# Performance work log

Hardware: AMD Instinct MI355X
Metric: run time of the kernel (lower is better)

The kernel has to match this reference:

```python
import jax, jax.numpy as jnp
import numpy as np

BLOCK = 128          # quantization block size
F8_MAX = 448.0       # max representable magnitude of float8_e4m3fn


def setup_inputs() -> dict:
    key = jax.random.key(0)
    k1, k2, k3 = jax.random.split(key, 3)
    M, K, N = 8192, 4096, 4096
    Kb, Nb = K // BLOCK, N // BLOCK
    x = jax.random.normal(k1, (M, K), jnp.float32)
    # weight stored as fp8-representable values (simulated with f32 container)
    weight = jax.random.normal(k2, (N, K), jnp.float32)
    # per 128x128-block weight dequant scales (positive, small, like amax/448)
    weight_scale = jax.random.uniform(k3, (Nb, Kb), jnp.float32, 0.5, 1.5) * 0.01
    return {"x": x, "weight": weight, "weight_scale": weight_scale}


def _act_quant(x):
    """fp8_blockwise_act_quant: per-(row, 128-block) scale = amax/448, cast to e4m3."""
    M, K = x.shape
    Kb = K // BLOCK
    xb = x.reshape(M, Kb, BLOCK)
    amax = jnp.max(jnp.abs(xb), axis=-1, keepdims=True)            # [M, Kb, 1]
    scale = jnp.maximum(amax, 1e-12) / F8_MAX                      # [M, Kb, 1]
    xq = (xb / scale).astype(jnp.float8_e4m3fn).astype(jnp.float32)
    return xq, scale


def reference(x, weight, weight_scale):
    # ---- activation blockwise fp8 quant ----
    xq, x_scale = _act_quant(x)                                    # [M,Kb,B], [M,Kb,1]
    M, Kb, _ = xq.shape
    K = Kb * BLOCK
    x_deq = (xq * x_scale).reshape(M, K)                           # dequantized activations

    # ---- weight blockwise fp8 dequant (weight stored as fp8 values) ----
    N = weight.shape[0]
    Nb = N // BLOCK
    wq = weight.astype(jnp.float8_e4m3fn).astype(jnp.float32)      # fp8 storage
    w_deq = (wq.reshape(Nb, BLOCK, Kb, BLOCK)
             * weight_scale[:, None, :, None]).reshape(N, K)

    # ---- scaled GEMM: y = x_deq @ w_deq^T (bias is None) ----
    return x_deq @ w_deq.T                                         # [M, N]
```

## Files before the change

### kernel.cpp

```cpp
#include <hip/hip_runtime.h>


typedef int   v4i __attribute__((ext_vector_type(4)));
typedef int   v8i __attribute__((ext_vector_type(8)));
typedef float v4f __attribute__((ext_vector_type(4)));

constexpr int M  = 8192;
constexpr int K  = 4096;
constexpr int N  = 4096;
constexpr int KB = K / 128;
constexpr int NB = N / 128;

constexpr int XBLOCKS = (M * KB * 8) / 256;
constexpr int WBLOCKS = (int)(((long long)N * K / 16) / 256);

#define GLOBAL_AS __attribute__((address_space(1)))
#define LDS_AS    __attribute__((address_space(3)))

__device__ __forceinline__ void async16(const void* g, void* l) {
  __builtin_amdgcn_global_load_lds((const GLOBAL_AS void*)g, (LDS_AS void*)l, 16, 0, 0);
}


__global__ __launch_bounds__(256) void quant_fused_kernel(
    const float* __restrict__ x, const float* __restrict__ w,
    unsigned char* __restrict__ xq, unsigned char* __restrict__ wq,
    float* __restrict__ xs_t ) {
  const int tid = threadIdx.x;
  if (blockIdx.x < XBLOCKS) {
    const long long blk = ((long long)blockIdx.x * 256 + tid) >> 3;
    const int s = tid & 7;
    const int m  = (int)(blk >> 5);
    const int kb = (int)(blk & (KB - 1));

    const float4* px = (const float4*)(x + blk * 128 + s * 16);
    float4 v0 = px[0], v1 = px[1], v2 = px[2], v3 = px[3];

    float ax = 0.f;
#define AMAX4(v) ax = fmaxf(ax, fmaxf(fmaxf(fabsf(v.x), fabsf(v.y)), fmaxf(fabsf(v.z), fabsf(v.w))))
    AMAX4(v0); AMAX4(v1); AMAX4(v2); AMAX4(v3);
#undef AMAX4
#pragma unroll
    for (int d = 4; d >= 1; d >>= 1) ax = fmaxf(ax, __shfl_xor(ax, d, 8));
    const float scale = fmaxf(ax, 1e-12f) / 448.0f;

    int p0 = 0, p1 = 0, p2 = 0, p3 = 0;
    p0 = __builtin_amdgcn_cvt_pk_fp8_f32(v0.x / scale, v0.y / scale, p0, false);
    p0 = __builtin_amdgcn_cvt_pk_fp8_f32(v0.z / scale, v0.w / scale, p0, true);
    p1 = __builtin_amdgcn_cvt_pk_fp8_f32(v1.x / scale, v1.y / scale, p1, false);
    p1 = __builtin_amdgcn_cvt_pk_fp8_f32(v1.z / scale, v1.w / scale, p1, true);
    p2 = __builtin_amdgcn_cvt_pk_fp8_f32(v2.x / scale, v2.y / scale, p2, false);
    p2 = __builtin_amdgcn_cvt_pk_fp8_f32(v2.z / scale, v2.w / scale, p2, true);
    p3 = __builtin_amdgcn_cvt_pk_fp8_f32(v3.x / scale, v3.y / scale, p3, false);
    p3 = __builtin_amdgcn_cvt_pk_fp8_f32(v3.z / scale, v3.w / scale, p3, true);

    const int q = s >> 1, j = s & 1, rr = m & 15;
    const long long base = ((long long)(m >> 4) * KB + kb) * 2048;
    *(v4i*)(xq + base + j * 1024 + (q * 16 + rr) * 16) = (v4i){p0, p1, p2, p3};

    if (s == 0) xs_t[(long long)kb * M + m] = scale;
  } else {
    const long long t = (long long)(blockIdx.x - XBLOCKS) * 256 + tid;
    const int grp = (int)(t >> 7);
    const int idx = (int)(t & 127);
    const int l = idx >> 1, j = idx & 1;
    const int nf = grp >> 5, kb = grp & (KB - 1);
    const int n = nf * 16 + (l & 15);
    const int k = kb * 128 + (l >> 4) * 32 + j * 16;

    const float4* pw = (const float4*)(w + (long long)n * K + k);
    float4 v0 = pw[0], v1 = pw[1], v2 = pw[2], v3 = pw[3];
    int p0 = 0, p1 = 0, p2 = 0, p3 = 0;
    p0 = __builtin_amdgcn_cvt_pk_fp8_f32(v0.x, v0.y, p0, false);
    p0 = __builtin_amdgcn_cvt_pk_fp8_f32(v0.z, v0.w, p0, true);
    p1 = __builtin_amdgcn_cvt_pk_fp8_f32(v1.x, v1.y, p1, false);
    p1 = __builtin_amdgcn_cvt_pk_fp8_f32(v1.z, v1.w, p1, true);
    p2 = __builtin_amdgcn_cvt_pk_fp8_f32(v2.x, v2.y, p2, false);
    p2 = __builtin_amdgcn_cvt_pk_fp8_f32(v2.z, v2.w, p2, true);
    p3 = __builtin_amdgcn_cvt_pk_fp8_f32(v3.x, v3.y, p3, false);
    p3 = __builtin_amdgcn_cvt_pk_fp8_f32(v3.z, v3.w, p3, true);
    *(v4i*)(wq + (long long)grp * 2048 + j * 1024 + l * 16) = (v4i){p0, p1, p2, p3};
  }
}

__global__ __launch_bounds__(512, 2) void gemm_fp8_kernel(
    const unsigned char* __restrict__ xq, const unsigned char* __restrict__ wq,
    const float* __restrict__ xs_t ,
    const float* __restrict__ wscale ,
    float* __restrict__ out) {
  __shared__ unsigned char Asm[2][16 * 2048];
  __shared__ unsigned char Bsm[2][16 * 2048];
  __shared__ float Ssm[2][256];

  const int tid   = threadIdx.x;
  const int ntile = blockIdx.x;
  const int mtile = blockIdx.y;
  const int wave  = tid >> 6;
  const int lane  = tid & 63;
  const int wm = wave >> 2, wn = wave & 3;
  const int l15 = lane & 15, quad = lane >> 4;

  const float wsv = wscale[(ntile * 2 + (wn >> 1)) * KB + (lane & 31)];

  const unsigned char* pa0 =
      xq + ((long long)(mtile * 16 + wave * 2) * KB) * 2048 + lane * 16;
  const unsigned char* pb0 =
      wq + ((long long)(ntile * 16 + wave * 2) * KB) * 2048 + lane * 16;
  const char* ps0 = (const char*)(xs_t + (long long)mtile * 256) + lane * 16;

  auto STAGE = [&](int nbuf, int kbi) {
    const long long koff = (long long)kbi * 2048;
#pragma unroll
    for (int t = 0; t < 4; ++t)
      async16(pa0 + koff + (long long)(t >> 1) * (KB * 2048) + (t & 1) * 1024,
              &Asm[nbuf][(wave * 2 + (t >> 1)) * 2048 + (t & 1) * 1024]);
#pragma unroll
    for (int t = 0; t < 4; ++t)
      async16(pb0 + koff + (long long)(t >> 1) * (KB * 2048) + (t & 1) * 1024,
              &Bsm[nbuf][(wave * 2 + (t >> 1)) * 2048 + (t & 1) * 1024]);
    if (wave == 0) async16(ps0 + (long long)kbi * (M * 4), &Ssm[nbuf][0]);
  };

  v4f acc[8][4];
#pragma unroll
  for (int f = 0; f < 8; ++f)
#pragma unroll
    for (int g = 0; g < 4; ++g) acc[f][g] = (v4f){0.f, 0.f, 0.f, 0.f};

  const v4f z = (v4f){0.f, 0.f, 0.f, 0.f};

  STAGE(0, 0);

#pragma unroll 1
  for (int kb = 0; kb < KB; ++kb) {
    const int cur = kb & 1;
    if (kb < KB - 1) {
      STAGE(cur ^ 1, kb + 1);
      if (wave == 0) asm volatile("s_waitcnt vmcnt(9)" ::: "memory");
      else           asm volatile("s_waitcnt vmcnt(8)" ::: "memory");
    } else {
      asm volatile("s_waitcnt vmcnt(0)" ::: "memory");
    }
    __builtin_amdgcn_s_barrier();
    asm volatile("" ::: "memory");
    __builtin_amdgcn_sched_barrier(0);

    const float ws =
        __uint_as_float(__builtin_amdgcn_readlane(__float_as_uint(wsv), kb));

    v8i b[4];
#pragma unroll
    for (int g = 0; g < 4; ++g) {
      const unsigned char* pb = Bsm[cur] + (wn * 4 + g) * 2048 + lane * 16;
      v4i lo = *(const v4i*)pb;
      v4i hi = *(const v4i*)(pb + 1024);
      b[g][0] = lo[0]; b[g][1] = lo[1]; b[g][2] = lo[2]; b[g][3] = lo[3];
      b[g][4] = hi[0]; b[g][5] = hi[1]; b[g][6] = hi[2]; b[g][7] = hi[3];
    }

#pragma unroll
    for (int f = 0; f < 8; ++f) {
      const unsigned char* pa = Asm[cur] + (wm * 8 + f) * 2048 + lane * 16;
      v4i lo = *(const v4i*)pa;
      v4i hi = *(const v4i*)(pa + 1024);
      v8i a;
      a[0] = lo[0]; a[1] = lo[1]; a[2] = lo[2]; a[3] = lo[3];
      a[4] = hi[0]; a[5] = hi[1]; a[6] = hi[2]; a[7] = hi[3];
      const v4f sxr = *(const v4f*)&Ssm[cur][wm * 128 + f * 16 + quad * 4];
      const v4f s = sxr * ws;
      v4f p[4];
      __builtin_amdgcn_s_setprio(1);
#pragma unroll
      for (int g = 0; g < 4; ++g) {
        p[g] = __builtin_amdgcn_mfma_scale_f32_16x16x128_f8f6f4(
            a, b[g], z, 0, 0, 0, 0x7f7f7f7f, 0, 0x7f7f7f7f);
      }
      __builtin_amdgcn_s_setprio(0);
#pragma unroll
      for (int g = 0; g < 4; ++g) acc[f][g] += s * p[g];
    }
    __syncthreads();
  }

#pragma unroll
  for (int f = 0; f < 8; ++f) {
#pragma unroll
    for (int r = 0; r < 4; ++r) {
      const long long row = mtile * 256 + wm * 128 + f * 16 + quad * 4 + r;
      float* po = out + row * N + ntile * 256 + wn * 64 + l15;
#pragma unroll
      for (int g = 0; g < 4; ++g) po[g * 16] = acc[f][g][r];
    }
  }
}

extern "C" void kernel_launch(void* const* d_in, const int* in_sizes, int n_in,
                              void* d_out, int out_size, void* d_ws, size_t ws_size,
                              hipStream_t stream) {
  const float* x   = (const float*)d_in[0];
  const float* w   = (const float*)d_in[1];
  const float* wsc = (const float*)d_in[2];
  float* out = (float*)d_out;

  unsigned char* ws = (unsigned char*)d_ws;
  unsigned char* xq = ws;
  unsigned char* wq = ws + (size_t)M * K;
  float* xs_t = (float*)(ws + (size_t)M * K + (size_t)N * K);

  quant_fused_kernel<<<XBLOCKS + WBLOCKS, 256, 0, stream>>>(x, w, xq, wq, xs_t);
  gemm_fp8_kernel<<<dim3(N / 256, M / 256), 512, 0, stream>>>(xq, wq, xs_t, wsc, out);
}
```

Before: 422.9 us.

## Split GEMM k-step into four barrier-separated phases interleaving prefetch with MFMA clusters

The main loop of the fp8 GEMM is rebuilt as four phases per k-block. Each phase issues one slice of the next stage's async global-to-LDS loads, loads a smaller set of A/B fragments from LDS, and runs an 8-MFMA cluster. The goal is to spread memory traffic across the compute and lower the register footprint (4 A fragments and 2 B fragments held at once instead of all 4 B fragments). In exchange it adds several extra workgroup barriers and lgkmcnt(0) waits per iteration, which could serialize the waves.

Measured after the change: 948.3 us. 2.24x slower.

```diff
diff --git a/kernel.cpp b/kernel.cpp
--- a/kernel.cpp
+++ b/kernel.cpp
@@ -108,78 +108,128 @@
       wq + ((long long)(ntile * 16 + wave * 2) * KB) * 2048 + lane * 16;
   const char* ps0 = (const char*)(xs_t + (long long)mtile * 256) + lane * 16;
 
-  auto STAGE = [&](int nbuf, int kbi) {
-    const long long koff = (long long)kbi * 2048;
-#pragma unroll
-    for (int t = 0; t < 4; ++t)
-      async16(pa0 + koff + (long long)(t >> 1) * (KB * 2048) + (t & 1) * 1024,
-              &Asm[nbuf][(wave * 2 + (t >> 1)) * 2048 + (t & 1) * 1024]);
-#pragma unroll
-    for (int t = 0; t < 4; ++t)
-      async16(pb0 + koff + (long long)(t >> 1) * (KB * 2048) + (t & 1) * 1024,
-              &Bsm[nbuf][(wave * 2 + (t >> 1)) * 2048 + (t & 1) * 1024]);
-    if (wave == 0) async16(ps0 + (long long)kbi * (M * 4), &Ssm[nbuf][0]);
-  };
+#define STAGE_A(nbuf, kbi, pair)                                               \
+  {                                                                            \
+    const long long koff_ = (long long)(kbi)*2048;                             \
+    async16(pa0 + koff_ + (long long)(pair) * (KB * 2048),                     \
+            &Asm[nbuf][(wave * 2 + (pair)) * 2048]);                           \
+    async16(pa0 + koff_ + (long long)(pair) * (KB * 2048) + 1024,              \
+            &Asm[nbuf][(wave * 2 + (pair)) * 2048 + 1024]);                    \
+  }
+#define STAGE_B(nbuf, kbi, pair)                                               \
+  {                                                                            \
+    const long long koff_ = (long long)(kbi)*2048;                             \
+    async16(pb0 + koff_ + (long long)(pair) * (KB * 2048),                     \
+            &Bsm[nbuf][(wave * 2 + (pair)) * 2048]);                           \
+    async16(pb0 + koff_ + (long long)(pair) * (KB * 2048) + 1024,              \
+            &Bsm[nbuf][(wave * 2 + (pair)) * 2048 + 1024]);                    \
+  }
+#define STAGE_S(nbuf, kbi)                                                     \
+  async16(ps0 + (long long)(kbi) * (M * 4), &Ssm[nbuf][0])
+
+#define LDBF(g, dst)                                                           \
+  {                                                                            \
+    const unsigned char* pb_ = Bq + (wn * 4 + (g)) * 2048 + lane * 16;         \
+    v4i lo_ = *(const v4i*)pb_;                                                \
+    v4i hi_ = *(const v4i*)(pb_ + 1024);                                       \
+    dst[0] = lo_[0]; dst[1] = lo_[1]; dst[2] = lo_[2]; dst[3] = lo_[3];        \
+    dst[4] = hi_[0]; dst[5] = hi_[1]; dst[6] = hi_[2]; dst[7] = hi_[3];        \
+  }
+#define LDAF(f, dst)                                                           \
+  {                                                                            \
+    const unsigned char* pa_ = Aq + (wm * 8 + (f)) * 2048 + lane * 16;         \
+    v4i lo_ = *(const v4i*)pa_;                                                \
+    v4i hi_ = *(const v4i*)(pa_ + 1024);                                       \
+    dst[0] = lo_[0]; dst[1] = lo_[1]; dst[2] = lo_[2]; dst[3] = lo_[3];        \
+    dst[4] = hi_[0]; dst[5] = hi_[1]; dst[6] = hi_[2]; dst[7] = hi_[3];        \
+  }
+
+#define FENCE asm volatile("" ::: "memory")
+#define LGKM0_PIN                                                              \
+  asm volatile("s_waitcnt lgkmcnt(0)" ::: "memory");                           \
+  __builtin_amdgcn_sched_barrier(0)
+
+#define CLUSTER(FH, G0)                                                        \
+  {                                                                            \
+    __builtin_amdgcn_s_setprio(1);                                             \
+    _Pragma("unroll") for (int fl = 0; fl < 4; ++fl) {                         \
+      v4f p0_ = __builtin_amdgcn_mfma_scale_f32_16x16x128_f8f6f4(              \
+          a4[fl], b2[0], zf, 0, 0, 0, 0x7f7f7f7f, 0, 0x7f7f7f7f);              \
+      v4f p1_ = __builtin_amdgcn_mfma_scale_f32_16x16x128_f8f6f4(              \
+          a4[fl], b2[1], zf, 0, 0, 0, 0x7f7f7f7f, 0, 0x7f7f7f7f);              \
+      acc[(FH)*4 + fl][(G0)] += sx4[fl] * p0_;                                 \
+      acc[(FH)*4 + fl][(G0) + 1] += sx4[fl] * p1_;                             \
+    }                                                                          \
+    __builtin_amdgcn_s_setprio(0);                                             \
+  }
 
   v4f acc[8][4];
 #pragma unroll
   for (int f = 0; f < 8; ++f)
 #pragma unroll
     for (int g = 0; g < 4; ++g) acc[f][g] = (v4f){0.f, 0.f, 0.f, 0.f};
-
-  const v4f z = (v4f){0.f, 0.f, 0.f, 0.f};
-
-  STAGE(0, 0);
+  const v4f zf = (v4f){0.f, 0.f, 0.f, 0.f};
+
+  STAGE_A(0, 0, 0); STAGE_A(0, 0, 1);
+  STAGE_B(0, 0, 0); STAGE_B(0, 0, 1);
+  if (wave == 0) STAGE_S(0, 0);
+
+  v8i a4[4], b2[2];
+  v4f sx4[4];
 
 #pragma unroll 1
   for (int kb = 0; kb < KB; ++kb) {
-    const int cur = kb & 1;
-    if (kb < KB - 1) {
-      STAGE(cur ^ 1, kb + 1);
-      if (wave == 0) asm volatile("s_waitcnt vmcnt(9)" ::: "memory");
-      else           asm volatile("s_waitcnt vmcnt(8)" ::: "memory");
-    } else {
-      asm volatile("s_waitcnt vmcnt(0)" ::: "memory");
-    }
-    __builtin_amdgcn_s_barrier();
-    asm volatile("" ::: "memory");
-    __builtin_amdgcn_sched_barrier(0);
-
+    const int cur = kb & 1, nxt = cur ^ 1;
+    const bool pref = (kb < KB - 1);
+    const unsigned char* Aq = Asm[cur];
+    const unsigned char* Bq = Bsm[cur];
     const float ws =
         __uint_as_float(__builtin_amdgcn_readlane(__float_as_uint(wsv), kb));
 
-    v8i b[4];
-#pragma unroll
-    for (int g = 0; g < 4; ++g) {
-      const unsigned char* pb = Bsm[cur] + (wn * 4 + g) * 2048 + lane * 16;
-      v4i lo = *(const v4i*)pb;
-      v4i hi = *(const v4i*)(pb + 1024);
-      b[g][0] = lo[0]; b[g][1] = lo[1]; b[g][2] = lo[2]; b[g][3] = lo[3];
-      b[g][4] = hi[0]; b[g][5] = hi[1]; b[g][6] = hi[2]; b[g][7] = hi[3];
-    }
-
-#pragma unroll
-    for (int f = 0; f < 8; ++f) {
-      const unsigned char* pa = Asm[cur] + (wm * 8 + f) * 2048 + lane * 16;
-      v4i lo = *(const v4i*)pa;
-      v4i hi = *(const v4i*)(pa + 1024);
-      v8i a;
-      a[0] = lo[0]; a[1] = lo[1]; a[2] = lo[2]; a[3] = lo[3];
-      a[4] = hi[0]; a[5] = hi[1]; a[6] = hi[2]; a[7] = hi[3];
-      const v4f sxr = *(const v4f*)&Ssm[cur][wm * 128 + f * 16 + quad * 4];
-      const v4f s = sxr * ws;
-      v4f p[4];
-      __builtin_amdgcn_s_setprio(1);
-#pragma unroll
-      for (int g = 0; g < 4; ++g) {
-        p[g] = __builtin_amdgcn_mfma_scale_f32_16x16x128_f8f6f4(
-            a, b[g], z, 0, 0, 0, 0x7f7f7f7f, 0, 0x7f7f7f7f);
-      }
-      __builtin_amdgcn_s_setprio(0);
-#pragma unroll
-      for (int g = 0; g < 4; ++g) acc[f][g] += s * p[g];
-    }
-    __syncthreads();
+    if (pref) STAGE_A(nxt, kb + 1, 0);
+    if (pref) asm volatile("s_waitcnt vmcnt(2)" ::: "memory");
+    else      asm volatile("s_waitcnt vmcnt(0)" ::: "memory");
+    __builtin_amdgcn_s_barrier();
+    FENCE; __builtin_amdgcn_sched_barrier(0);
+    LDBF(0, b2[0]); LDBF(1, b2[1]);
+#pragma unroll
+    for (int fl = 0; fl < 4; ++fl) LDAF(fl, a4[fl]);
+#pragma unroll
+    for (int fl = 0; fl < 4; ++fl)
+      sx4[fl] = *(const v4f*)&Ssm[cur][wm * 128 + fl * 16 + quad * 4];
+    LGKM0_PIN;
+#pragma unroll
+    for (int fl = 0; fl < 4; ++fl) sx4[fl] *= ws;
+    CLUSTER(0, 0);
+    FENCE; __builtin_amdgcn_s_barrier();
+
+    if (pref) STAGE_A(nxt, kb + 1, 1);
+    LDBF(2, b2[0]); LDBF(3, b2[1]);
+    FENCE; __builtin_amdgcn_s_barrier();
+    LGKM0_PIN;
+    CLUSTER(0, 2);
+    FENCE; __builtin_amdgcn_s_barrier();
+
+    if (pref) STAGE_B(nxt, kb + 1, 0);
+#pragma unroll
+    for (int fl = 0; fl < 4; ++fl) LDAF(4 + fl, a4[fl]);
+#pragma unroll
+    for (int fl = 0; fl < 4; ++fl)
+      sx4[fl] = *(const v4f*)&Ssm[cur][wm * 128 + (4 + fl) * 16 + quad * 4];
+    FENCE; __builtin_amdgcn_s_barrier();
+    LGKM0_PIN;
+#pragma unroll
+    for (int fl = 0; fl < 4; ++fl) sx4[fl] *= ws;
+    CLUSTER(1, 2);
+    FENCE; __builtin_amdgcn_s_barrier();
+
+    if (pref) STAGE_B(nxt, kb + 1, 1);
+    if (pref && wave == 0) STAGE_S(nxt, kb + 1);
+    LDBF(0, b2[0]); LDBF(1, b2[1]);
+    FENCE; __builtin_amdgcn_s_barrier();
+    LGKM0_PIN;
+    CLUSTER(1, 0);
+    FENCE; __builtin_amdgcn_s_barrier();
   }
 
 #pragma unroll
```
